# Kernel optimization log

Measured on AMD Instinct MI355X. Metric: run time of the kernel, lower is better.

Reference implementation:

```python
import jax, jax.numpy as jnp
import numpy as np

# OPT-1.3b-like attention dims
B, S, E, NH, HD = 1, 2048, 2048, 32, 64
Q_BITS, R_BITS, BASE_GS, R_GS = 1, 3, 16, 16


def quotrem_fake_quantize(x, q_bits=Q_BITS, r_bits=R_BITS, base_gs=BASE_GS, r_gs=R_GS):
    r_max = 2 ** (r_bits - 1) - 1
    r_min = -r_max - 1
    eps = 1e-8
    shape = x.shape
    H = shape[-1]
    xg = x.reshape(shape[:-1] + (H // base_gs, base_gs))  # [..., G_base, base_gs]
    max_abs = jnp.maximum(jnp.max(jnp.abs(xg), axis=-1, keepdims=True), eps)
    if q_bits == 1:
        log2_max = jnp.log2(max_abs)
        base_floor = jnp.exp2(jnp.floor(log2_max))
        base_ceil = jnp.exp2(jnp.ceil(log2_max))
        base = jnp.where(jnp.abs(max_abs - base_floor) <= jnp.abs(base_ceil - max_abs),
                         base_floor, base_ceil)
        base = jnp.clip(base, 1.0, 128.0)
        max_pos = jnp.max(xg, axis=-1, keepdims=True)
        min_val = jnp.min(xg, axis=-1, keepdims=True)
        sign_flag = jnp.where(jnp.abs(max_pos) >= jnp.abs(min_val), 1.0, -1.0)
        q = (xg * sign_flag >= base / 2.0).astype(x.dtype)
        q_scaled = q * sign_flag * base
    else:
        q_max = 2 ** (q_bits - 1) - 1
        threshold = max_abs / q_max
        base = jnp.full_like(threshold, 64.0)
        for b in (32.0, 16.0, 8.0, 4.0, 2.0):
            base = jnp.where(threshold <= b, jnp.full_like(threshold, b), base)
        q = jnp.clip(jnp.round(xg / base), -q_max, q_max)
        q_scaled = q * base
    r = (xg - q_scaled).reshape(shape)
    rg = r.reshape(shape[:-1] + (H // r_gs, r_gs))  # [..., G_r, r_gs]
    max_abs_r = jnp.maximum(jnp.max(jnp.abs(rg), axis=-1, keepdims=True), eps)
    scale_r = max_abs_r / r_max
    r_q = jnp.clip(jnp.round(rg / scale_r), r_min, r_max)
    r_dq = (r_q * scale_r).reshape(shape)
    return q_scaled.reshape(shape) + r_dq


def setup_inputs() -> dict:
    key = jax.random.key(0)
    ks = jax.random.split(key, 9)
    w = lambda k: jax.random.normal(k, (E, E), dtype=jnp.float32) * 0.02
    b = lambda k: jax.random.normal(k, (E,), dtype=jnp.float32) * 0.02
    return {
        "hidden_states": jax.random.normal(ks[0], (B, S, E), dtype=jnp.float32),
        "Wq": w(ks[1]), "bq": b(ks[2]),
        "Wk": w(ks[3]), "bk": b(ks[4]),
        "Wv": w(ks[5]), "bv": b(ks[6]),
        "Wo": w(ks[7]), "bo": b(ks[8]),
    }


def reference(hidden_states, Wq, bq, Wk, bk, Wv, bv, Wo, bo):
    scaling = HD ** -0.5
    heads = lambda x: x.reshape(B, S, NH, HD).transpose(0, 2, 1, 3)  # [B,NH,S,HD]
    q = heads((hidden_states @ Wq.T + bq) * scaling)
    k = quotrem_fake_quantize(heads(hidden_states @ Wk.T + bk))
    v = quotrem_fake_quantize(heads(hidden_states @ Wv.T + bv))
    scores = jnp.einsum('bhqd,bhkd->bhqk', q, k)
    idx = jnp.arange(S)
    scores = jnp.where(idx[:, None] >= idx[None, :], scores, -jnp.inf)  # causal
    attn = jax.nn.softmax(scores, axis=-1)
    out = jnp.einsum('bhqk,bhkd->bhqd', attn, v).transpose(0, 2, 1, 3).reshape(B, S, E)
    return out @ Wo.T + bo
```

## Files before the change

kernel.cpp:

```cpp
#include <hip/hip_runtime.h>
#include <math.h>

#define SEQ 2048
#define EMB 2048
#define NHEAD 32
#define HDIM 64

typedef unsigned short u16;
typedef _Float16 half8 __attribute__((ext_vector_type(8)));
typedef _Float16 half4 __attribute__((ext_vector_type(4)));
typedef __attribute__((ext_vector_type(4))) float floatx4;

__device__ __forceinline__ floatx4 mfma_f16(half8 a, half8 b, floatx4 c) {
    return __builtin_amdgcn_mfma_f32_16x16x32_f16(a, b, c, 0, 0, 0);
}
__device__ __forceinline__ void load16(const u16* g, u16* l) {
    __builtin_amdgcn_global_load_lds(
        (const __attribute__((address_space(1))) unsigned int*)g,
        (__attribute__((address_space(3))) unsigned int*)l, 16, 0, 0);
}
__device__ __forceinline__ u16 h2u(_Float16 h) { return *reinterpret_cast<u16*>(&h); }

__global__ __launch_bounds__(256)
void cvt4(const float* __restrict__ X0, u16* __restrict__ Y0,
          const float* __restrict__ X1, u16* __restrict__ Y1,
          const float* __restrict__ X2, u16* __restrict__ Y2,
          const float* __restrict__ X3, u16* __restrict__ Y3)
{
    const float* Xs[4] = {X0, X1, X2, X3};
    u16* Ys[4] = {Y0, Y1, Y2, Y3};
    const float* X = Xs[blockIdx.y];
    u16* Y = Ys[blockIdx.y];
    const int i = (blockIdx.x * 256 + threadIdx.x) * 4;
    float4 v = *reinterpret_cast<const float4*>(X + i);
    half4 hv;
    hv.x = (_Float16)v.x; hv.y = (_Float16)v.y;
    hv.z = (_Float16)v.z; hv.w = (_Float16)v.w;
    *reinterpret_cast<half4*>(Y + i) = hv;
}

__global__ __launch_bounds__(512, 2)
void gemm256(const u16* __restrict__ A,
             const u16* __restrict__ B0, const u16* __restrict__ B1,
             const u16* __restrict__ B2,
             const float* __restrict__ bk, const float* __restrict__ bv,
             const float* __restrict__ bq,
             float* __restrict__ F0, float* __restrict__ F1,
             u16* __restrict__ Qb)
{
    __shared__ __align__(16) u16 As[2][256 * 64];
    __shared__ __align__(16) u16 Bs[2][256 * 64];

    const int tid = threadIdx.x;
    const int w = tid >> 6, lane = tid & 63;
    const int wm = w >> 2, wn = w & 3;
    const int quad = lane >> 4, colk = lane & 15;
    const int lrow = lane >> 3, lphy = lane & 7;
    const int lsLog = (lphy - lrow) & 7;
    const int bn = blockIdx.x, bm = blockIdx.y, z = blockIdx.z;

    const u16* Bg  = (z == 0) ? B0 : (z == 1) ? B1 : B2;
    const u16* Ag  = A  + (size_t)(bm * 256 + lrow) * EMB + lsLog * 8;
    const u16* Bgp = Bg + (size_t)(bn * 256 + lrow) * EMB + lsLog * 8;

    const int kp0 = ((quad + colk) & 7) * 8;
    const int kp1 = ((quad + 4 + colk) & 7) * 8;
    int arow[8], brow[4];
    #pragma unroll
    for (int i = 0; i < 8; ++i) arow[i] = (wm * 128 + 16 * i + colk) * 64;
    #pragma unroll
    for (int j = 0; j < 4; ++j) brow[j] = (wn * 64 + 16 * j + colk) * 64;

    floatx4 acc[8][4];
    #pragma unroll
    for (int i = 0; i < 8; ++i)
        #pragma unroll
        for (int j = 0; j < 4; ++j) acc[i][j] = (floatx4){0.f, 0.f, 0.f, 0.f};

    half8 af[4][2], bf0[2][2], bf1[2][2];

#define STAGE_A(MQ, BUF, KT) {                                                \
    _Pragma("unroll") for (int p_ = 0; p_ < 2; ++p_) {                        \
        const int r0_ = 128 * p_ + (MQ) * 64 + w * 8;                         \
        load16(Ag + (size_t)r0_ * EMB + (KT), &As[BUF][r0_ * 64 + lane * 8]); \
    } }
#define STAGE_B(NQ, BUF, KT) {                                                \
    _Pragma("unroll") for (int p_ = 0; p_ < 2; ++p_) {                        \
        const int b_ = w + 8 * p_;                                            \
        const int r0_ = 64 * (b_ >> 2) + (NQ) * 32 + (b_ & 3) * 8;            \
        load16(Bgp + (size_t)r0_ * EMB + (KT), &Bs[BUF][r0_ * 64 + lane * 8]);\
    } }
#define READ_A(MQ, BUF)                                                       \
    _Pragma("unroll") for (int ii_ = 0; ii_ < 4; ++ii_) {                     \
        const u16* ap_ = &As[BUF][arow[4*(MQ)+ii_]];                          \
        af[ii_][0] = *reinterpret_cast<const half8*>(ap_ + kp0);              \
        af[ii_][1] = *reinterpret_cast<const half8*>(ap_ + kp1);              \
    }
#define READ_B(NQ, BUF, DST)                                                  \
    _Pragma("unroll") for (int jj_ = 0; jj_ < 2; ++jj_) {                     \
        const u16* bp_ = &Bs[BUF][brow[2*(NQ)+jj_]];                          \
        DST[jj_][0] = *reinterpret_cast<const half8*>(bp_ + kp0);             \
        DST[jj_][1] = *reinterpret_cast<const half8*>(bp_ + kp1);             \
    }
#define VM6 asm volatile("s_waitcnt vmcnt(6)" ::: "memory");
#define VM8 asm volatile("s_waitcnt vmcnt(8)" ::: "memory");
#define VM0 asm volatile("s_waitcnt vmcnt(0)" ::: "memory");

#define PHASE(READS, STAGE, MQ, NQ, BF, GUARD, NEEDLGKM) {                    \
    READS                                                                     \
    STAGE                                                                     \
    __builtin_amdgcn_s_barrier();                                             \
    if (NEEDLGKM) {                                                           \
        asm volatile("s_waitcnt lgkmcnt(0)" ::: "memory");                    \
        __builtin_amdgcn_sched_barrier(0);                                    \
    }                                                                         \
    __builtin_amdgcn_s_setprio(1);                                            \
    _Pragma("unroll") for (int ii = 0; ii < 4; ++ii)                          \
        _Pragma("unroll") for (int jj = 0; jj < 2; ++jj) {                    \
            acc[4*(MQ)+ii][2*(NQ)+jj] =                                       \
                mfma_f16(af[ii][0], BF[jj][0], acc[4*(MQ)+ii][2*(NQ)+jj]);    \
            acc[4*(MQ)+ii][2*(NQ)+jj] =                                       \
                mfma_f16(af[ii][1], BF[jj][1], acc[4*(MQ)+ii][2*(NQ)+jj]);    \
        }                                                                     \
    __builtin_amdgcn_s_setprio(0);                                            \
    GUARD                                                                     \
    __builtin_amdgcn_s_barrier();                                             \
    __builtin_amdgcn_sched_barrier(0);                                        \
}

    STAGE_A(0, 0, 0)  STAGE_B(0, 0, 0)  STAGE_B(1, 0, 0)  STAGE_A(1, 0, 0)
    STAGE_A(0, 1, 64) STAGE_B(0, 1, 64) STAGE_B(1, 1, 64) STAGE_A(1, 1, 64)
    asm volatile("s_waitcnt vmcnt(8)" ::: "memory");
    __builtin_amdgcn_s_barrier();
    __builtin_amdgcn_sched_barrier(0);

    #pragma unroll 1
    for (int it = 0; it < 15; ++it) {
        const int k2 = (2 * it + 2) * 64;
        const int k3 = (2 * it + 3) * 64;
        PHASE(READ_A(0,0) READ_B(0,0,bf0), {},                0,0,bf0, {},  1)
        PHASE(READ_B(1,0,bf1),             STAGE_A(0,0,k2),   0,1,bf1, {},  1)
        PHASE(READ_A(1,0),                 STAGE_B(0,0,k2),   1,1,bf1, {},  1)
        PHASE({},                          STAGE_B(1,0,k2),   1,0,bf0, VM6, 0)
        PHASE(READ_A(0,1) READ_B(0,1,bf0), STAGE_A(1,0,k2),   0,0,bf0, {},  1)
        PHASE(READ_B(1,1,bf1),             STAGE_A(0,1,k3),   0,1,bf1, {},  1)
        PHASE(READ_A(1,1),                 STAGE_B(0,1,k3),   1,1,bf1, {},  1)
        PHASE({},    STAGE_B(1,1,k3) STAGE_A(1,1,k3),         1,0,bf0, VM8, 0)
    }
    PHASE(READ_A(0,0) READ_B(0,0,bf0), {}, 0,0,bf0, {},  1)
    PHASE(READ_B(1,0,bf1),             {}, 0,1,bf1, {},  1)
    PHASE(READ_A(1,0),                 {}, 1,1,bf1, {},  1)
    PHASE({},                          {}, 1,0,bf0, VM0, 0)
    PHASE(READ_A(0,1) READ_B(0,1,bf0), {}, 0,0,bf0, {},  1)
    PHASE(READ_B(1,1,bf1),             {}, 0,1,bf1, {},  1)
    PHASE(READ_A(1,1),                 {}, 1,1,bf1, {},  1)
    PHASE({},                          {}, 1,0,bf0, {},  0)

#undef STAGE_A
#undef STAGE_B
#undef READ_A
#undef READ_B
#undef VM6
#undef VM8
#undef VM0
#undef PHASE

    const float* bias = (z == 0) ? bk : (z == 1) ? bv : bq;
    #pragma unroll
    for (int i = 0; i < 8; ++i) {
        const int row = bm * 256 + wm * 128 + 16 * i + 4 * quad;
        #pragma unroll
        for (int j = 0; j < 4; ++j) {
            const int col = bn * 256 + wn * 64 + 16 * j + colk;
            const float bb = bias[col];
            #pragma unroll
            for (int r = 0; r < 4; ++r) {
                const size_t idx = (size_t)(row + r) * EMB + col;
                if (z == 2)
                    ((_Float16*)Qb)[idx] = (_Float16)((acc[i][j][r] + bb) * 0.125f);
                else
                    ((z == 0) ? F0 : F1)[idx] = acc[i][j][r] + bb;
            }
        }
    }
}

__global__ __launch_bounds__(256)
void gemm16(const u16* __restrict__ A,
            const u16* __restrict__ B0, const u16* __restrict__ B1,
            const u16* __restrict__ B2,
            const float* __restrict__ bk, const float* __restrict__ bv,
            const float* __restrict__ bq,
            float* __restrict__ F0, float* __restrict__ F1,
            u16* __restrict__ Qb)
{
    __shared__ __align__(16) u16 As[128 * 64];
    __shared__ __align__(16) u16 Bs[128 * 64];

    const int tid = threadIdx.x;
    const int w = tid >> 6, lane = tid & 63;
    const int quad = lane >> 4, colk = lane & 15;
    const int bn = blockIdx.x, bm = blockIdx.y, z = blockIdx.z;
    const int wm = (w & 1) * 64, wn = (w >> 1) * 64;

    const u16* Bg = (z == 0) ? B0 : (z == 1) ? B1 : B2;

    const int srow = tid >> 3, sphy = tid & 7;
    const int sLog = (sphy - srow) & 7;
    size_t agof[4], bgof[4];
    int ldst[4];
    #pragma unroll
    for (int p = 0; p < 4; ++p) {
        const int row = srow + 32 * p;
        agof[p] = (size_t)(bm * 128 + row) * EMB + sLog * 8;
        bgof[p] = (size_t)(bn * 128 + row) * EMB + sLog * 8;
        ldst[p] = (tid + 256 * p) * 8;
    }

    const int aoct0 = ((quad + colk) & 7) * 8;
    const int aoct1 = ((quad + 4 + colk) & 7) * 8;

    floatx4 acc[4][4];
    #pragma unroll
    for (int i = 0; i < 4; ++i)
        #pragma unroll
        for (int j = 0; j < 4; ++j) acc[i][j] = (floatx4){0.f, 0.f, 0.f, 0.f};

    for (int kt = 0; kt < 2048; kt += 64) {
        __syncthreads();
        #pragma unroll
        for (int p = 0; p < 4; ++p) {
            load16(A  + agof[p] + kt, As + ldst[p]);
            load16(Bg + bgof[p] + kt, Bs + ldst[p]);
        }
        __syncthreads();

        half8 a0[4], a1[4], b0[4], b1[4];
        #pragma unroll
        for (int i = 0; i < 4; ++i) {
            a0[i] = *reinterpret_cast<const half8*>(&As[(wm + 16*i + colk) * 64 + aoct0]);
            a1[i] = *reinterpret_cast<const half8*>(&As[(wm + 16*i + colk) * 64 + aoct1]);
        }
        #pragma unroll
        for (int j = 0; j < 4; ++j) {
            b0[j] = *reinterpret_cast<const half8*>(&Bs[(wn + 16*j + colk) * 64 + aoct0]);
            b1[j] = *reinterpret_cast<const half8*>(&Bs[(wn + 16*j + colk) * 64 + aoct1]);
        }
        #pragma unroll
        for (int i = 0; i < 4; ++i)
            #pragma unroll
            for (int j = 0; j < 4; ++j) {
                acc[i][j] = mfma_f16(a0[i], b0[j], acc[i][j]);
                acc[i][j] = mfma_f16(a1[i], b1[j], acc[i][j]);
            }
    }

    const float* bias = (z == 0) ? bk : (z == 1) ? bv : bq;
    #pragma unroll
    for (int i = 0; i < 4; ++i) {
        const int row = bm * 128 + wm + 16*i + 4*quad;
        #pragma unroll
        for (int j = 0; j < 4; ++j) {
            const int col = bn * 128 + wn + 16*j + colk;
            const float bv2 = bias[col];
            #pragma unroll
            for (int r = 0; r < 4; ++r) {
                const size_t idx = (size_t)(row + r) * EMB + col;
                if (z == 2)
                    ((_Float16*)Qb)[idx] = (_Float16)((acc[i][j][r] + bv2) * 0.125f);
                else
                    ((z == 0) ? F0 : F1)[idx] = acc[i][j][r] + bv2;
            }
        }
    }
}

__device__ __forceinline__ void quotrem16(float* x)
{
    float maxabs = 1e-8f, maxpos = -INFINITY, minval = INFINITY;
    #pragma unroll
    for (int i = 0; i < 16; ++i) {
        maxabs = fmaxf(maxabs, fabsf(x[i]));
        maxpos = fmaxf(maxpos, x[i]);
        minval = fminf(minval, x[i]);
    }
    const float lg = log2f(maxabs);
    const float bfl = exp2f(floorf(lg));
    const float bcl = exp2f(ceilf(lg));
    float base = (fabsf(maxabs - bfl) <= fabsf(bcl - maxabs)) ? bfl : bcl;
    base = fminf(fmaxf(base, 1.0f), 128.0f);
    const float sgn = (fabsf(maxpos) >= fabsf(minval)) ? 1.0f : -1.0f;
    const float hb = 0.5f * base, sb = sgn * base;

    float qs[16], r[16], maxr = 1e-8f;
    #pragma unroll
    for (int i = 0; i < 16; ++i) {
        qs[i] = (x[i] * sgn >= hb) ? sb : 0.0f;
        r[i]  = x[i] - qs[i];
        maxr  = fmaxf(maxr, fabsf(r[i]));
    }
    const float scale = maxr / 3.0f;
    #pragma unroll
    for (int i = 0; i < 16; ++i) {
        float rq = rintf(r[i] / scale);
        rq = fminf(fmaxf(rq, -4.0f), 3.0f);
        x[i] = qs[i] + rq * scale;
    }
}

__global__ __launch_bounds__(256)
void quant_kv(const float* __restrict__ FK, u16* __restrict__ Kb,
              const float* __restrict__ FV, u16* __restrict__ Vt,
              const float* __restrict__ Wo, u16* __restrict__ Wo16)
{
    __shared__ u16 T[64 * 264];
    const int bid = blockIdx.x, t = threadIdx.x;

    if (bid >= 1280) {
        const int i = ((bid - 1280) * 256 + t) * 4;
        float4 v = *reinterpret_cast<const float4*>(Wo + i);
        half4 hv;
        hv.x = (_Float16)v.x; hv.y = (_Float16)v.y;
        hv.z = (_Float16)v.z; hv.w = (_Float16)v.w;
        *reinterpret_cast<half4*>(Wo16 + i) = hv;
        return;
    }

    if (bid < 1024) {
        const int g = bid * 256 + t;
        const float* p = FK + (size_t)g * 16;
        float x[16];
        #pragma unroll
        for (int i = 0; i < 16; i += 4)
            *reinterpret_cast<float4*>(&x[i]) = *reinterpret_cast<const float4*>(p + i);
        quotrem16(x);
        _Float16* o = (_Float16*)Kb + (size_t)g * 16;
        #pragma unroll
        for (int i = 0; i < 16; ++i) o[i] = (_Float16)x[i];
        return;
    }

    const int l = bid - 1024;
    const int sb = l >> 5, h = l & 31;
    const float* src = FV + (size_t)(sb * 256 + t) * EMB + h * HDIM;

    #pragma unroll
    for (int g4 = 0; g4 < 4; ++g4) {
        float x[16];
        #pragma unroll
        for (int i = 0; i < 16; i += 4)
            *reinterpret_cast<float4*>(&x[i]) =
                *reinterpret_cast<const float4*>(src + g4 * 16 + i);
        quotrem16(x);
        #pragma unroll
        for (int i = 0; i < 16; ++i)
            T[(g4 * 16 + i) * 264 + t] = h2u((_Float16)x[i]);
    }
    __syncthreads();

    const int d = t >> 2, seg = t & 3;
    u16* dst = Vt + (size_t)(h * HDIM + d) * SEQ + sb * 256 + seg * 64;
    #pragma unroll
    for (int jj = 0; jj < 8; ++jj)
        *reinterpret_cast<half8*>(dst + jj * 8) =
            *reinterpret_cast<const half8*>(&T[d * 264 + seg * 64 + jj * 8]);
}

__global__ __launch_bounds__(256)
void flash128(const u16* __restrict__ Qb, const u16* __restrict__ Kb,
              const u16* __restrict__ Vt, u16* __restrict__ Ob)
{
    __shared__ __align__(16) u16 Ks[128 * 64];
    __shared__ __align__(16) u16 Vs[64 * 128];
    __shared__ __align__(16) u16 Ps[64 * 136];

    const int tid = threadIdx.x;
    const int w = tid >> 6, lane = tid & 63;
    const int quad = lane >> 4, colk = lane & 15;
    const int id = blockIdx.x;
    const int h = (id & 7) * 4 + ((id >> 3) & 3);
    const int pairb = id >> 5;

    int krow[4], koff[4], vd[4], voff[4];
    #pragma unroll
    for (int p = 0; p < 4; ++p) {
        const int c = tid + p * 256;
        krow[p] = c >> 3;
        koff[p] = (((c & 7) - krow[p]) & 7) * 8;
        vd[p]   = c >> 4;
        voff[p] = (((c & 15) - vd[p]) & 15) * 8;
    }
    const int ldb0 = w * 512;
    const int kp0 = ((quad + colk) & 7) * 8;
    const int kp1 = ((quad + 4 + colk) & 7) * 8;

    #pragma unroll
    for (int pass = 0; pass < 2; ++pass) {
        const int qt = pass ? (31 - pairb) : pairb;
        const int nw = (qt + 2) >> 1;
        const int qrow_g = qt * 64 + 16 * w + colk;

        __syncthreads();
        #pragma unroll
        for (int p = 0; p < 2; ++p) {
            const int c = tid + p * 256, row = c >> 3, cq = c & 7;
            *reinterpret_cast<half8*>(&Ps[row * 136 + cq * 8]) =
                *reinterpret_cast<const half8*>(&Qb[(size_t)(qt * 64 + row) * EMB + h * HDIM + cq * 8]);
        }
        __syncthreads();
        const half8 qb0 = *reinterpret_cast<const half8*>(&Ps[(16*w + colk) * 136 + quad * 8]);
        const half8 qb1 = *reinterpret_cast<const half8*>(&Ps[(16*w + colk) * 136 + 32 + quad * 8]);

        floatx4 o[4];
        #pragma unroll
        for (int t = 0; t < 4; ++t) o[t] = (floatx4){0.f, 0.f, 0.f, 0.f};
        float lsum = 0.f;

        for (int kw = 0; kw < nw; ++kw) {
            __syncthreads();
            #pragma unroll
            for (int p = 0; p < 4; ++p) {
                load16(Kb + (size_t)(kw * 128 + krow[p]) * EMB + h * HDIM + koff[p],
                       Ks + p * 2048 + ldb0);
                load16(Vt + (size_t)(h * HDIM + vd[p]) * SEQ + kw * 128 + voff[p],
                       Vs + p * 2048 + ldb0);
            }
            __syncthreads();

            floatx4 s[8];
            #pragma unroll
            for (int t = 0; t < 8; ++t) {
                const half8 kb0 = *reinterpret_cast<const half8*>(&Ks[(16*t + colk) * 64 + kp0]);
                const half8 kb1 = *reinterpret_cast<const half8*>(&Ks[(16*t + colk) * 64 + kp1]);
                floatx4 zz = (floatx4){0.f, 0.f, 0.f, 0.f};
                zz = mfma_f16(kb0, qb0, zz);
                s[t] = mfma_f16(kb1, qb1, zz);
            }
            if (kw == nw - 1) {
                #pragma unroll
                for (int t = 0; t < 8; ++t)
                    #pragma unroll
                    for (int r = 0; r < 4; ++r)
                        if (kw * 128 + 16*t + 4*quad + r > qrow_g) s[t][r] = -INFINITY;
            }

            #pragma unroll
            for (int t = 0; t < 8; ++t) {
                half4 pw;
                float pv0 = __expf(s[t][0] - 4.0f), pv1 = __expf(s[t][1] - 4.0f);
                float pv2 = __expf(s[t][2] - 4.0f), pv3 = __expf(s[t][3] - 4.0f);
                lsum += (pv0 + pv1) + (pv2 + pv3);
                pw.x = (_Float16)pv0; pw.y = (_Float16)pv1;
                pw.z = (_Float16)pv2; pw.w = (_Float16)pv3;
                *reinterpret_cast<half4*>(&Ps[(16*w + colk) * 136 + 16*t + 4*quad]) = pw;
            }

            half8 pa[4];
            #pragma unroll
            for (int seg = 0; seg < 4; ++seg)
                pa[seg] = *reinterpret_cast<const half8*>(&Ps[(16*w + colk) * 136 + seg * 32 + quad * 8]);
            #pragma unroll
            for (int t = 0; t < 4; ++t) {
                #pragma unroll
                for (int seg = 0; seg < 4; ++seg) {
                    const int vp = ((4*seg + quad + colk) & 15) * 8;
                    const half8 vb = *reinterpret_cast<const half8*>(&Vs[(16*t + colk) * 128 + vp]);
                    o[t] = mfma_f16(pa[seg], vb, o[t]);
                }
            }
        }

        lsum += __shfl_xor(lsum, 16, 64);
        lsum += __shfl_xor(lsum, 32, 64);

        float invr[4];
        #pragma unroll
        for (int r = 0; r < 4; ++r) invr[r] = 1.0f / __shfl(lsum, 4*quad + r, 64);
        #pragma unroll
        for (int t = 0; t < 4; ++t)
            #pragma unroll
            for (int r = 0; r < 4; ++r) {
                const int row = qt * 64 + 16*w + 4*quad + r;
                ((_Float16*)Ob)[(size_t)row * EMB + h * HDIM + 16*t + colk] =
                    (_Float16)(o[t][r] * invr[r]);
            }
    }
}

extern "C" void kernel_launch(void* const* d_in, const int* in_sizes, int n_in,
                              void* d_out, int out_size, void* d_ws, size_t ws_size,
                              hipStream_t stream)
{
    const float* hidden = (const float*)d_in[0];
    const float* Wq = (const float*)d_in[1];
    const float* bq = (const float*)d_in[2];
    const float* Wk = (const float*)d_in[3];
    const float* bk = (const float*)d_in[4];
    const float* Wv = (const float*)d_in[5];
    const float* bv = (const float*)d_in[6];
    const float* Wo = (const float*)d_in[7];
    const float* bo = (const float*)d_in[8];
    float* out = (float*)d_out;

    char* ws = (char*)d_ws;
    const size_t MB = 1024 * 1024;
    u16*   H16  = (u16*)(ws);
    u16*   Wk16 = (u16*)(ws + 8 * MB);
    u16*   Wv16 = (u16*)(ws + 16 * MB);
    float* FK   = (float*)(ws + 24 * MB);
    float* FV   = (float*)(ws + 40 * MB);
    u16*   Qbuf = (u16*)(ws + 56 * MB);
    u16*   Kbuf = (u16*)(ws + 8 * MB);
    u16*   Vtb  = (u16*)(ws + 16 * MB);
    u16*   Wo16 = (u16*)(ws);
    u16*   Obuf = (u16*)(ws + 24 * MB);
    u16*   Wq16 = (u16*)d_out;

    const dim3 cb(256);
    float* nilf = nullptr; u16* nil16 = nullptr;

    hipLaunchKernelGGL(cvt4, dim3(4096, 4), cb, 0, stream,
                       hidden, H16, Wk, Wk16, Wv, Wv16, Wq, Wq16);
    hipLaunchKernelGGL(gemm256, dim3(8, 8, 3), dim3(512), 0, stream,
                       H16, Wk16, Wv16, Wq16, bk, bv, bq, FK, FV, Qbuf);
    hipLaunchKernelGGL(quant_kv, dim3(1280 + 4096), cb, 0, stream,
                       FK, Kbuf, FV, Vtb, Wo, Wo16);
    hipLaunchKernelGGL(flash128, dim3(512), cb, 0, stream,
                       Qbuf, Kbuf, Vtb, Obuf);
    hipLaunchKernelGGL(gemm16, dim3(16, 16, 1), cb, 0, stream,
                       Obuf, Wo16, nil16, nil16, bo, nilf, nilf,
                       out, nilf, nil16);
}
```

Measured before the change: 287.0 us.

## Double-buffer GEMM register fragments to prefetch LDS reads one phase ahead

The 256x256 QKV projection GEMM now keeps two sets of A and B register fragments. Each phase reads the LDS tiles for the next phase while the current phase's MFMAs run, and the explicit lgkmcnt(0) wait before each MFMA block is removed. The global-to-LDS staging order and the vmcnt guard thresholds are reworked to match. This aims to hide LDS read latency behind matrix math, but it raises register pressure under the 512x2 launch bounds and depends on the compiler inserting correct LDS waits.

```diff
diff --git a/kernel.cpp b/kernel.cpp
--- a/kernel.cpp
+++ b/kernel.cpp
@@ -41,8 +41,8 @@
 
 __global__ __launch_bounds__(512, 2)
 void gemm256(const u16* __restrict__ A,
-             const u16* __restrict__ B0, const u16* __restrict__ B1,
-             const u16* __restrict__ B2,
+             const u16* __restrict__ B0g, const u16* __restrict__ B1g,
+             const u16* __restrict__ B2g,
              const float* __restrict__ bk, const float* __restrict__ bv,
              const float* __restrict__ bq,
              float* __restrict__ F0, float* __restrict__ F1,
@@ -59,7 +59,7 @@
     const int lsLog = (lphy - lrow) & 7;
     const int bn = blockIdx.x, bm = blockIdx.y, z = blockIdx.z;
 
-    const u16* Bg  = (z == 0) ? B0 : (z == 1) ? B1 : B2;
+    const u16* Bg  = (z == 0) ? B0g : (z == 1) ? B1g : B2g;
     const u16* Ag  = A  + (size_t)(bm * 256 + lrow) * EMB + lsLog * 8;
     const u16* Bgp = Bg + (size_t)(bn * 256 + lrow) * EMB + lsLog * 8;
 
@@ -77,7 +77,7 @@
         #pragma unroll
         for (int j = 0; j < 4; ++j) acc[i][j] = (floatx4){0.f, 0.f, 0.f, 0.f};
 
-    half8 af[4][2], bf0[2][2], bf1[2][2];
+    half8 A0f[4][2], A1f[4][2], B0f[2][2], B1f[2][2];
 
 #define STAGE_A(MQ, BUF, KT) {                                                \
     _Pragma("unroll") for (int p_ = 0; p_ < 2; ++p_) {                        \
@@ -90,78 +90,76 @@
         const int r0_ = 64 * (b_ >> 2) + (NQ) * 32 + (b_ & 3) * 8;            \
         load16(Bgp + (size_t)r0_ * EMB + (KT), &Bs[BUF][r0_ * 64 + lane * 8]);\
     } }
-#define READ_A(MQ, BUF)                                                       \
+#define READ_A(DST, MQ, BUF)                                                  \
     _Pragma("unroll") for (int ii_ = 0; ii_ < 4; ++ii_) {                     \
         const u16* ap_ = &As[BUF][arow[4*(MQ)+ii_]];                          \
-        af[ii_][0] = *reinterpret_cast<const half8*>(ap_ + kp0);              \
-        af[ii_][1] = *reinterpret_cast<const half8*>(ap_ + kp1);              \
-    }
-#define READ_B(NQ, BUF, DST)                                                  \
+        DST[ii_][0] = *reinterpret_cast<const half8*>(ap_ + kp0);             \
+        DST[ii_][1] = *reinterpret_cast<const half8*>(ap_ + kp1);             \
+    }
+#define READ_B(DST, NQ, BUF)                                                  \
     _Pragma("unroll") for (int jj_ = 0; jj_ < 2; ++jj_) {                     \
         const u16* bp_ = &Bs[BUF][brow[2*(NQ)+jj_]];                          \
         DST[jj_][0] = *reinterpret_cast<const half8*>(bp_ + kp0);             \
         DST[jj_][1] = *reinterpret_cast<const half8*>(bp_ + kp1);             \
     }
-#define VM6 asm volatile("s_waitcnt vmcnt(6)" ::: "memory");
-#define VM8 asm volatile("s_waitcnt vmcnt(8)" ::: "memory");
-#define VM0 asm volatile("s_waitcnt vmcnt(0)" ::: "memory");
-
-#define PHASE(READS, STAGE, MQ, NQ, BF, GUARD, NEEDLGKM) {                    \
-    READS                                                                     \
-    STAGE                                                                     \
+#define VM10 asm volatile("s_waitcnt vmcnt(10)" ::: "memory");
+#define VM6  asm volatile("s_waitcnt vmcnt(6)" ::: "memory");
+#define VM0  asm volatile("s_waitcnt vmcnt(0)" ::: "memory");
+
+#define PHASE(RPRE, STG, MQ, NQ, AF, BF, RPOST, GRD) {                        \
+    RPRE                                                                      \
+    STG                                                                       \
     __builtin_amdgcn_s_barrier();                                             \
-    if (NEEDLGKM) {                                                           \
-        asm volatile("s_waitcnt lgkmcnt(0)" ::: "memory");                    \
-        __builtin_amdgcn_sched_barrier(0);                                    \
-    }                                                                         \
     __builtin_amdgcn_s_setprio(1);                                            \
     _Pragma("unroll") for (int ii = 0; ii < 4; ++ii)                          \
         _Pragma("unroll") for (int jj = 0; jj < 2; ++jj) {                    \
             acc[4*(MQ)+ii][2*(NQ)+jj] =                                       \
-                mfma_f16(af[ii][0], BF[jj][0], acc[4*(MQ)+ii][2*(NQ)+jj]);    \
+                mfma_f16(AF[ii][0], BF[jj][0], acc[4*(MQ)+ii][2*(NQ)+jj]);    \
             acc[4*(MQ)+ii][2*(NQ)+jj] =                                       \
-                mfma_f16(af[ii][1], BF[jj][1], acc[4*(MQ)+ii][2*(NQ)+jj]);    \
+                mfma_f16(AF[ii][1], BF[jj][1], acc[4*(MQ)+ii][2*(NQ)+jj]);    \
         }                                                                     \
     __builtin_amdgcn_s_setprio(0);                                            \
-    GUARD                                                                     \
+    RPOST                                                                     \
+    GRD                                                                       \
     __builtin_amdgcn_s_barrier();                                             \
     __builtin_amdgcn_sched_barrier(0);                                        \
 }
 
-    STAGE_A(0, 0, 0)  STAGE_B(0, 0, 0)  STAGE_B(1, 0, 0)  STAGE_A(1, 0, 0)
-    STAGE_A(0, 1, 64) STAGE_B(0, 1, 64) STAGE_B(1, 1, 64) STAGE_A(1, 1, 64)
+    STAGE_A(0, 0, 0)  STAGE_B(0, 0, 0)  STAGE_A(1, 0, 0)  STAGE_B(1, 0, 0)
+    STAGE_A(0, 1, 64) STAGE_B(0, 1, 64) STAGE_A(1, 1, 64) STAGE_B(1, 1, 64)
     asm volatile("s_waitcnt vmcnt(8)" ::: "memory");
     __builtin_amdgcn_s_barrier();
     __builtin_amdgcn_sched_barrier(0);
+    READ_A(A0f, 0, 0) READ_B(B0f, 0, 0) READ_B(B1f, 1, 0)
 
     #pragma unroll 1
     for (int it = 0; it < 15; ++it) {
         const int k2 = (2 * it + 2) * 64;
         const int k3 = (2 * it + 3) * 64;
-        PHASE(READ_A(0,0) READ_B(0,0,bf0), {},                0,0,bf0, {},  1)
-        PHASE(READ_B(1,0,bf1),             STAGE_A(0,0,k2),   0,1,bf1, {},  1)
-        PHASE(READ_A(1,0),                 STAGE_B(0,0,k2),   1,1,bf1, {},  1)
-        PHASE({},                          STAGE_B(1,0,k2),   1,0,bf0, VM6, 0)
-        PHASE(READ_A(0,1) READ_B(0,1,bf0), STAGE_A(1,0,k2),   0,0,bf0, {},  1)
-        PHASE(READ_B(1,1,bf1),             STAGE_A(0,1,k3),   0,1,bf1, {},  1)
-        PHASE(READ_A(1,1),                 STAGE_B(0,1,k3),   1,1,bf1, {},  1)
-        PHASE({},    STAGE_B(1,1,k3) STAGE_A(1,1,k3),         1,0,bf0, VM8, 0)
-    }
-    PHASE(READ_A(0,0) READ_B(0,0,bf0), {}, 0,0,bf0, {},  1)
-    PHASE(READ_B(1,0,bf1),             {}, 0,1,bf1, {},  1)
-    PHASE(READ_A(1,0),                 {}, 1,1,bf1, {},  1)
-    PHASE({},                          {}, 1,0,bf0, VM0, 0)
-    PHASE(READ_A(0,1) READ_B(0,1,bf0), {}, 0,0,bf0, {},  1)
-    PHASE(READ_B(1,1,bf1),             {}, 0,1,bf1, {},  1)
-    PHASE(READ_A(1,1),                 {}, 1,1,bf1, {},  1)
-    PHASE({},                          {}, 1,0,bf0, {},  0)
+        PHASE(READ_A(A1f,1,0), {},                               0,0, A0f,B0f, {},                VM10)
+        PHASE({},              STAGE_A(0,0,k2) STAGE_B(0,0,k2),  0,1, A0f,B1f, {},                VM10)
+        PHASE(READ_A(A0f,0,1), STAGE_A(1,0,k2),                  1,1, A1f,B1f, {},                VM6)
+        PHASE(READ_B(B1f,1,1), STAGE_B(1,0,k2),                  1,0, A1f,B0f, READ_B(B0f,0,1),   VM10)
+        PHASE(READ_A(A1f,1,1), STAGE_A(0,1,k3),                  0,0, A0f,B0f, {},                VM10)
+        PHASE({},              STAGE_B(0,1,k3),                  0,1, A0f,B1f, {},                VM10)
+        PHASE(READ_A(A0f,0,0), STAGE_A(1,1,k3),                  1,1, A1f,B1f, {},                VM6)
+        PHASE(READ_B(B1f,1,0), STAGE_B(1,1,k3),                  1,0, A1f,B0f, READ_B(B0f,0,0),   VM10)
+    }
+    PHASE(READ_A(A1f,1,0), {}, 0,0, A0f,B0f, {},              {})
+    PHASE({},              {}, 0,1, A0f,B1f, {},              VM6)
+    PHASE(READ_A(A0f,0,1), {}, 1,1, A1f,B1f, {},              VM0)
+    PHASE(READ_B(B1f,1,1), {}, 1,0, A1f,B0f, READ_B(B0f,0,1), {})
+    PHASE(READ_A(A1f,1,1), {}, 0,0, A0f,B0f, {},              {})
+    PHASE({},              {}, 0,1, A0f,B1f, {},              {})
+    PHASE({},              {}, 1,1, A1f,B1f, {},              {})
+    PHASE({},              {}, 1,0, A1f,B0f, {},              {})
 
 #undef STAGE_A
 #undef STAGE_B
 #undef READ_A
 #undef READ_B
+#undef VM10
 #undef VM6
-#undef VM8
 #undef VM0
 #undef PHASE
 
```

After: 314.4 us. 1.1x slower.
